# Kernel optimization log

Measured on AMD Instinct MI355X. Metric: run time of the kernel, lower is better.

## Reference

```python
import jax, jax.numpy as jnp
import numpy as np

T, K, N, G = 8192, 1024, 2048, 8  # total_rows, k, n, num_groups


def setup_inputs() -> dict:
    key = jax.random.key(0)
    kA, kB, kO = jax.random.split(key, 3)
    A = jax.random.normal(kA, (T, K), dtype=jnp.float32)
    B = jax.random.normal(kB, (G, K, N), dtype=jnp.float32) * 0.02
    # monotonically increasing end-offsets; last offset covers all rows
    offsets = jnp.sort(jax.random.randint(kO, (G,), 1, T)).at[-1].set(T).astype(jnp.int32)
    return {"A": A, "B": B, "offsets": offsets}


def reference(A, B, offsets):
    """Grouped GEMM: rows A[offsets[g-1]:offsets[g]] are multiplied by B[g].

    Implemented jit-compatibly (offsets may be traced) by masking rows per
    group and accumulating disjoint contributions; the Python loop is over
    the small, static number of groups only.
    """
    num_groups = B.shape[0]
    total_rows = A.shape[0]
    # group id of each row: first offset strictly greater than row index
    gid = jnp.searchsorted(offsets, jnp.arange(total_rows), side="right")  # [T]
    out = jnp.zeros((total_rows, B.shape[2]), dtype=A.dtype)
    for g in range(num_groups):
        mask = (gid == g)[:, None]                      # [T,1] disjoint masks
        out = out + jnp.where(mask, A, 0.0) @ B[g]      # [T,n]
    return out
```

## Files before the change

### kernel.cpp

```cpp
#include <hip/hip_runtime.h>
#include <hip/hip_bf16.h>

#define T_ROWS 8192
#define K_DIM  1024
#define N_DIM  2048
#define G_NUM  8
#define CONVA_BLOCKS 2048
#define CONVB_BLOCKS 4096

typedef __attribute__((ext_vector_type(8))) short short8;
typedef __attribute__((ext_vector_type(4))) float v4f;

__device__ __forceinline__ unsigned short f2bf(float x) {
  unsigned int u = __builtin_bit_cast(unsigned int, x);
  u += 0x7fffu + ((u >> 16) & 1u);
  return (unsigned short)(u >> 16);
}
__device__ __forceinline__ unsigned int pk2(float a, float b) {
  return (unsigned int)f2bf(a) | ((unsigned int)f2bf(b) << 16);
}
__device__ __forceinline__ void async_cp16(const void* gsrc, void* ldst) {
  __builtin_amdgcn_global_load_lds(
      (const __attribute__((address_space(1))) void*)gsrc,
      (__attribute__((address_space(3))) void*)ldst, 16, 0, 0);
}

__global__ __launch_bounds__(256) void conv_fused(const float* __restrict__ A,
                                                  const float* __restrict__ B,
                                                  unsigned short* __restrict__ Ab,
                                                  unsigned short* __restrict__ Bt) {
  __shared__ float tile[64][65];
  const int bid = blockIdx.x;
  const int t = threadIdx.x;
  const int q3 = bid / 3, r3 = bid - q3 * 3;

  if (r3 == 0) {
    size_t idx = (size_t)q3 * 256 + t;
    const float4* src = (const float4*)A + idx * 4;
    float4 v0 = src[0], v1 = src[1], v2 = src[2], v3 = src[3];
    uint4 o0, o1;
    o0.x = pk2(v0.x, v0.y); o0.y = pk2(v0.z, v0.w);
    o0.z = pk2(v1.x, v1.y); o0.w = pk2(v1.z, v1.w);
    o1.x = pk2(v2.x, v2.y); o1.y = pk2(v2.z, v2.w);
    o1.z = pk2(v3.x, v3.y); o1.w = pk2(v3.z, v3.w);
    ((uint4*)Ab)[idx * 2]     = o0;
    ((uint4*)Ab)[idx * 2 + 1] = o1;
    return;
  }
  const int bidx = 2 * q3 + (r3 - 1);
  const int nt = bidx & 31;
  const int kt = (bidx >> 5) & 15;
  const int g  = bidx >> 9;
  const int c4 = t & 15;
  const int r  = t >> 4;

  const float* src = B + ((size_t)g * K_DIM + (size_t)kt * 64) * N_DIM + (size_t)nt * 64;
#pragma unroll
  for (int i = 0; i < 4; ++i) {
    int k = r + i * 16;
    float4 v = *(const float4*)(src + (size_t)k * N_DIM + c4 * 4);
    tile[k][c4 * 4 + 0] = v.x; tile[k][c4 * 4 + 1] = v.y;
    tile[k][c4 * 4 + 2] = v.z; tile[k][c4 * 4 + 3] = v.w;
  }
  __syncthreads();
  unsigned short* dst = Bt + ((size_t)g * N_DIM + (size_t)nt * 64) * K_DIM + (size_t)kt * 64;
#pragma unroll
  for (int i = 0; i < 2; ++i) {
    int idx = t + i * 256;
    int n = idx >> 3;
    int seg = idx & 7;
    unsigned int u0 = pk2(tile[seg * 8 + 0][n], tile[seg * 8 + 1][n]);
    unsigned int u1 = pk2(tile[seg * 8 + 2][n], tile[seg * 8 + 3][n]);
    unsigned int u2 = pk2(tile[seg * 8 + 4][n], tile[seg * 8 + 5][n]);
    unsigned int u3 = pk2(tile[seg * 8 + 6][n], tile[seg * 8 + 7][n]);
    uint4 o; o.x = u0; o.y = u1; o.z = u2; o.w = u3;
    *(uint4*)(dst + (size_t)n * K_DIM + seg * 8) = o;
  }
}

__global__ __launch_bounds__(256) void gemm_kernel(const unsigned short* __restrict__ Ab,
                                                   const unsigned short* __restrict__ Btb,
                                                   const int* __restrict__ offs,
                                                   float* __restrict__ out) {
  __shared__ unsigned short As[128 * 64];
  __shared__ unsigned short Bs[128 * 64];
  const int t = threadIdx.x;

  const int b = blockIdx.x;
  const int xcd = b & 7;
  const int j = b >> 3;
  const int mslot = xcd * 9 + (j >> 4);
  const int n0 = (j & 15) * 128;

  int prev = 0, cum = 0, row0 = 0, row_end = 0, g = 0, found = 0;
#pragma unroll
  for (int gg = 0; gg < G_NUM; ++gg) {
    int e = offs[gg];
    int tiles = (e - prev + 127) >> 7;
    if (!found && mslot < cum + tiles) {
      found = 1; g = gg; row0 = prev + (mslot - cum) * 128; row_end = e;
    }
    cum += tiles;
    prev = e;
  }
  if (!found) return;

  const int lane = t & 63;
  const int wv = t >> 6;
  const int wm = wv & 1;
  const int wn = wv >> 1;
  const int srcChunk = (t & 7) ^ ((t >> 3) & 7);

  const unsigned short* aSrc[4];
  const unsigned short* bSrc[4];
  char* aDst[4];
  char* bDst[4];
#pragma unroll
  for (int c = 0; c < 4; ++c) {
    int rl = c * 32 + (t >> 3);
    int rA = row0 + rl; if (rA > T_ROWS - 1) rA = T_ROWS - 1;
    aSrc[c] = Ab + (size_t)rA * K_DIM + srcChunk * 8;
    bSrc[c] = Btb + ((size_t)g * N_DIM + n0 + rl) * K_DIM + srcChunk * 8;
    aDst[c] = (char*)As + c * 4096 + t * 16;
    bDst[c] = (char*)Bs + c * 4096 + t * 16;
  }

  v4f acc[4][4];
#pragma unroll
  for (int i = 0; i < 4; ++i)
#pragma unroll
    for (int j2 = 0; j2 < 4; ++j2)
#pragma unroll
      for (int r = 0; r < 4; ++r) acc[i][j2][r] = 0.0f;

#pragma unroll
  for (int c = 0; c < 4; ++c) {
    async_cp16(aSrc[c], aDst[c]);
    async_cp16(bSrc[c], bDst[c]);
  }

  for (int k0 = 0; k0 < K_DIM; k0 += 64) {
    __syncthreads();
#pragma unroll
    for (int ks = 0; ks < 2; ++ks) {
      short8 a[4], bfr[4];
      int chBase = (lane >> 4) + ks * 4;
      int chPhys = chBase ^ (lane & 7);
#pragma unroll
      for (int im = 0; im < 4; ++im) {
        int row = wm * 64 + im * 16 + (lane & 15);
        a[im] = *(const short8*)((const char*)As + row * 128 + chPhys * 16);
      }
#pragma unroll
      for (int in = 0; in < 4; ++in) {
        int row = wn * 64 + in * 16 + (lane & 15);
        bfr[in] = *(const short8*)((const char*)Bs + row * 128 + chPhys * 16);
      }
#pragma unroll
      for (int im = 0; im < 4; ++im)
#pragma unroll
        for (int in = 0; in < 4; ++in)
          acc[im][in] = __builtin_amdgcn_mfma_f32_16x16x32_bf16(a[im], bfr[in], acc[im][in], 0, 0, 0);
    }
    if (k0 + 64 < K_DIM) {
      __syncthreads();
      int koff = k0 + 64;
#pragma unroll
      for (int c = 0; c < 4; ++c) {
        async_cp16(aSrc[c] + koff, aDst[c]);
        async_cp16(bSrc[c] + koff, bDst[c]);
      }
    }
  }

  const int colBase = n0 + wn * 64 + (lane & 15);
  const int rowBase = row0 + wm * 64 + ((lane >> 4) << 2);
#pragma unroll
  for (int im = 0; im < 4; ++im) {
#pragma unroll
    for (int in = 0; in < 4; ++in) {
      int c = colBase + in * 16;
#pragma unroll
      for (int r = 0; r < 4; ++r) {
        int rr = rowBase + im * 16 + r;
        if (rr < row_end) out[(size_t)rr * N_DIM + c] = acc[im][in][r];
      }
    }
  }
}

__global__ __launch_bounds__(256) void fallback_kernel(const float* __restrict__ A,
                                                       const float* __restrict__ B,
                                                       const int* __restrict__ offs,
                                                       float* __restrict__ out) {
  int r = blockIdx.y;
  int c = blockIdx.x * 256 + threadIdx.x;
  int g = 0;
#pragma unroll
  for (int i = 0; i < G_NUM; ++i) g += (offs[i] <= r);
  const float* a = A + (size_t)r * K_DIM;
  const float* b = B + (size_t)g * K_DIM * N_DIM + c;
  float s = 0.f;
  for (int k = 0; k < K_DIM; ++k) s += a[k] * b[(size_t)k * N_DIM];
  out[(size_t)r * N_DIM + c] = s;
}

extern "C" void kernel_launch(void* const* d_in, const int* in_sizes, int n_in,
                              void* d_out, int out_size, void* d_ws, size_t ws_size,
                              hipStream_t stream) {
  const float* A = (const float*)d_in[0];
  const float* B = (const float*)d_in[1];
  const int* offs = (const int*)d_in[2];
  float* out = (float*)d_out;

  size_t need = ((size_t)T_ROWS * K_DIM + (size_t)G_NUM * K_DIM * N_DIM) * 2;
  if (ws_size < need) {
    dim3 grid(N_DIM / 256, T_ROWS);
    fallback_kernel<<<grid, 256, 0, stream>>>(A, B, offs, out);
    return;
  }
  unsigned short* Ab = (unsigned short*)d_ws;
  unsigned short* Btb = Ab + (size_t)T_ROWS * K_DIM;

  conv_fused<<<CONVA_BLOCKS + CONVB_BLOCKS, 256, 0, stream>>>(A, B, Ab, Btb);
  gemm_kernel<<<8 * 9 * 16, 256, 0, stream>>>(Ab, Btb, offs, out);
}
```

Before: 188.1 us.

## Pipeline GEMM mainloop with 4-stage LDS ring of K=32 tiles

Replaces the single-buffered 64-wide K loop, which waited on each load and used two barriers per step, with a four-slot LDS ring of 32-wide K tiles. Three tiles are kept in flight, and waits use explicit vmcnt counts with one barrier per phase. The MFMA block is wrapped in setprio and sched_barrier so it overlaps the async global-to-LDS copies. The unswizzled 64-byte row layout may cause LDS bank conflicts, and the hand-counted vmcnt values must be exactly right for correctness.

New measurement: 193.0 us. 2.6% more time.

```diff
diff --git a/kernel.cpp b/kernel.cpp
--- a/kernel.cpp
+++ b/kernel.cpp
@@ -82,8 +82,7 @@
                                                    const unsigned short* __restrict__ Btb,
                                                    const int* __restrict__ offs,
                                                    float* __restrict__ out) {
-  __shared__ unsigned short As[128 * 64];
-  __shared__ unsigned short Bs[128 * 64];
+  __shared__ char lds[65536];
   const int t = threadIdx.x;
 
   const int b = blockIdx.x;
@@ -109,21 +108,20 @@
   const int wv = t >> 6;
   const int wm = wv & 1;
   const int wn = wv >> 1;
-  const int srcChunk = (t & 7) ^ ((t >> 3) & 7);
-
-  const unsigned short* aSrc[4];
-  const unsigned short* bSrc[4];
-  char* aDst[4];
-  char* bDst[4];
-#pragma unroll
-  for (int c = 0; c < 4; ++c) {
-    int rl = c * 32 + (t >> 3);
+
+  const int t4 = t & 3;
+  const int rq = t >> 2;
+  const unsigned short* aSrc[2];
+  const unsigned short* bSrc[2];
+#pragma unroll
+  for (int i = 0; i < 2; ++i) {
+    int rl = i * 64 + rq;
     int rA = row0 + rl; if (rA > T_ROWS - 1) rA = T_ROWS - 1;
-    aSrc[c] = Ab + (size_t)rA * K_DIM + srcChunk * 8;
-    bSrc[c] = Btb + ((size_t)g * N_DIM + n0 + rl) * K_DIM + srcChunk * 8;
-    aDst[c] = (char*)As + c * 4096 + t * 16;
-    bDst[c] = (char*)Bs + c * 4096 + t * 16;
-  }
+    aSrc[i] = Ab + (size_t)rA * K_DIM + t4 * 8;
+    bSrc[i] = Btb + ((size_t)g * N_DIM + n0 + rl) * K_DIM + t4 * 8;
+  }
+
+  const int rowb = (lane & 15) * 64 + ((lane >> 4) << 4);
 
   v4f acc[4][4];
 #pragma unroll
@@ -133,45 +131,74 @@
 #pragma unroll
       for (int r = 0; r < 4; ++r) acc[i][j2][r] = 0.0f;
 
-#pragma unroll
-  for (int c = 0; c < 4; ++c) {
-    async_cp16(aSrc[c], aDst[c]);
-    async_cp16(bSrc[c], bDst[c]);
-  }
-
-  for (int k0 = 0; k0 < K_DIM; k0 += 64) {
-    __syncthreads();
-#pragma unroll
-    for (int ks = 0; ks < 2; ++ks) {
-      short8 a[4], bfr[4];
-      int chBase = (lane >> 4) + ks * 4;
-      int chPhys = chBase ^ (lane & 7);
-#pragma unroll
-      for (int im = 0; im < 4; ++im) {
-        int row = wm * 64 + im * 16 + (lane & 15);
-        a[im] = *(const short8*)((const char*)As + row * 128 + chPhys * 16);
-      }
-#pragma unroll
-      for (int in = 0; in < 4; ++in) {
-        int row = wn * 64 + in * 16 + (lane & 15);
-        bfr[in] = *(const short8*)((const char*)Bs + row * 128 + chPhys * 16);
-      }
-#pragma unroll
-      for (int im = 0; im < 4; ++im)
-#pragma unroll
-        for (int in = 0; in < 4; ++in)
-          acc[im][in] = __builtin_amdgcn_mfma_f32_16x16x32_bf16(a[im], bfr[in], acc[im][in], 0, 0, 0);
-    }
-    if (k0 + 64 < K_DIM) {
-      __syncthreads();
-      int koff = k0 + 64;
-#pragma unroll
-      for (int c = 0; c < 4; ++c) {
-        async_cp16(aSrc[c] + koff, aDst[c]);
-        async_cp16(bSrc[c] + koff, bDst[c]);
-      }
-    }
-  }
+#define ISSUE_T(TILE, S2)                                                  \
+  do {                                                                     \
+    char* ad_ = (char*)lds + (S2) * 8192 + t * 16;                         \
+    char* bd_ = (char*)lds + 32768 + (S2) * 8192 + t * 16;                 \
+    async_cp16(aSrc[0] + (TILE) * 32, ad_);                                \
+    async_cp16(aSrc[1] + (TILE) * 32, ad_ + 4096);                         \
+    async_cp16(bSrc[0] + (TILE) * 32, bd_);                                \
+    async_cp16(bSrc[1] + (TILE) * 32, bd_ + 4096);                         \
+  } while (0)
+
+#define PHASE_T(S, TILE, VM)                                               \
+  do {                                                                     \
+    asm volatile("s_waitcnt vmcnt(" #VM ")" ::: "memory");                 \
+    __builtin_amdgcn_s_barrier();                                          \
+    __builtin_amdgcn_sched_barrier(0);                                     \
+    if ((TILE) >= 0) ISSUE_T(TILE, ((S) + 3) & 3);                         \
+    short8 a0_, a1_, a2_, a3_, b0_, b1_, b2_, b3_;                         \
+    {                                                                      \
+      const char* ab_ = (const char*)lds + (S) * 8192 + wm * 4096 + rowb;  \
+      const char* bb_ = (const char*)lds + 32768 + (S) * 8192 + wn * 4096 + rowb; \
+      a0_ = *(const short8*)(ab_);                                         \
+      a1_ = *(const short8*)(ab_ + 1024);                                  \
+      a2_ = *(const short8*)(ab_ + 2048);                                  \
+      a3_ = *(const short8*)(ab_ + 3072);                                  \
+      b0_ = *(const short8*)(bb_);                                         \
+      b1_ = *(const short8*)(bb_ + 1024);                                  \
+      b2_ = *(const short8*)(bb_ + 2048);                                  \
+      b3_ = *(const short8*)(bb_ + 3072);                                  \
+    }                                                                      \
+    __builtin_amdgcn_s_setprio(1);                                         \
+    acc[0][0] = __builtin_amdgcn_mfma_f32_16x16x32_bf16(a0_, b0_, acc[0][0], 0, 0, 0); \
+    acc[0][1] = __builtin_amdgcn_mfma_f32_16x16x32_bf16(a0_, b1_, acc[0][1], 0, 0, 0); \
+    acc[0][2] = __builtin_amdgcn_mfma_f32_16x16x32_bf16(a0_, b2_, acc[0][2], 0, 0, 0); \
+    acc[0][3] = __builtin_amdgcn_mfma_f32_16x16x32_bf16(a0_, b3_, acc[0][3], 0, 0, 0); \
+    acc[1][0] = __builtin_amdgcn_mfma_f32_16x16x32_bf16(a1_, b0_, acc[1][0], 0, 0, 0); \
+    acc[1][1] = __builtin_amdgcn_mfma_f32_16x16x32_bf16(a1_, b1_, acc[1][1], 0, 0, 0); \
+    acc[1][2] = __builtin_amdgcn_mfma_f32_16x16x32_bf16(a1_, b2_, acc[1][2], 0, 0, 0); \
+    acc[1][3] = __builtin_amdgcn_mfma_f32_16x16x32_bf16(a1_, b3_, acc[1][3], 0, 0, 0); \
+    acc[2][0] = __builtin_amdgcn_mfma_f32_16x16x32_bf16(a2_, b0_, acc[2][0], 0, 0, 0); \
+    acc[2][1] = __builtin_amdgcn_mfma_f32_16x16x32_bf16(a2_, b1_, acc[2][1], 0, 0, 0); \
+    acc[2][2] = __builtin_amdgcn_mfma_f32_16x16x32_bf16(a2_, b2_, acc[2][2], 0, 0, 0); \
+    acc[2][3] = __builtin_amdgcn_mfma_f32_16x16x32_bf16(a2_, b3_, acc[2][3], 0, 0, 0); \
+    acc[3][0] = __builtin_amdgcn_mfma_f32_16x16x32_bf16(a3_, b0_, acc[3][0], 0, 0, 0); \
+    acc[3][1] = __builtin_amdgcn_mfma_f32_16x16x32_bf16(a3_, b1_, acc[3][1], 0, 0, 0); \
+    acc[3][2] = __builtin_amdgcn_mfma_f32_16x16x32_bf16(a3_, b2_, acc[3][2], 0, 0, 0); \
+    acc[3][3] = __builtin_amdgcn_mfma_f32_16x16x32_bf16(a3_, b3_, acc[3][3], 0, 0, 0); \
+    __builtin_amdgcn_s_setprio(0);                                         \
+    __builtin_amdgcn_sched_barrier(0);                                     \
+  } while (0)
+
+  ISSUE_T(0, 0);
+  ISSUE_T(1, 1);
+  ISSUE_T(2, 2);
+
+#pragma unroll 1
+  for (int tb = 0; tb < 28; tb += 4) {
+    PHASE_T(0, tb + 3, 8);
+    PHASE_T(1, tb + 4, 8);
+    PHASE_T(2, tb + 5, 8);
+    PHASE_T(3, tb + 6, 8);
+  }
+  PHASE_T(0, 31, 8);
+  PHASE_T(1, -1, 8);
+  PHASE_T(2, -1, 4);
+  PHASE_T(3, -1, 0);
+
+#undef PHASE_T
+#undef ISSUE_T
 
   const int colBase = n0 + wn * 64 + (lane & 15);
   const int rowBase = row0 + wm * 64 + ((lane >> 4) << 2);
```
